# Kernel tuning notes

Measured on AMD Instinct MI355X. Metric: run time of the kernel, lower is better.

The kernel has to match this reference:

```python
import jax, jax.numpy as jnp
import numpy as np

N_PTS0 = 32   # sample points per line
N_PTS1 = 8    # after maxpool1d (kernel/stride = 4)
DIM_LOI = 128
DIM_FC = 1024
TOPK = 300
HW = 128
NLINES = 20000
NLAB = 3


def setup_inputs() -> dict:
    key = jax.random.key(0)
    ks = jax.random.split(key, 10)
    jloc = jax.random.uniform(ks[0], (1, HW, HW), dtype=jnp.float32)
    joff = jax.random.uniform(ks[1], (2, HW, HW), dtype=jnp.float32)
    loi_features = jax.random.normal(ks[2], (DIM_LOI, HW, HW), dtype=jnp.float32)
    edge_idx = jax.random.randint(ks[3], (NLINES, 2), 0, TOPK, dtype=jnp.int32)
    W1 = jax.random.normal(ks[4], (DIM_LOI * N_PTS1, DIM_FC), dtype=jnp.float32) * 0.02
    b1 = jnp.zeros((DIM_FC,), jnp.float32)
    W2 = jax.random.normal(ks[5], (DIM_FC, DIM_FC), dtype=jnp.float32) * 0.02
    b2 = jnp.zeros((DIM_FC,), jnp.float32)
    W3 = jax.random.normal(ks[6], (DIM_FC, NLAB), dtype=jnp.float32) * 0.02
    b3 = jnp.zeros((NLAB,), jnp.float32)
    return {"jloc": jloc, "joff": joff, "loi_features": loi_features,
            "edge_idx": edge_idx, "W1": W1, "b1": b1, "W2": W2, "b2": b2,
            "W3": W3, "b3": b3}


def reference(jloc, joff, loi_features, edge_idx, W1, b1, W2, b2, W3, b3):
    C, h, w = loi_features.shape
    # --- NMS: 3x3 max_pool2d, keep only local maxima ---
    ap = jax.lax.reduce_window(jloc, -jnp.inf, jax.lax.max,
                               (1, 3, 3), (1, 1, 1), 'SAME')
    jloc_nms = jloc * (jloc == ap).astype(jloc.dtype)
    # --- top-k junction decoding (joff_pred = sigmoid(joff) - 0.5) ---
    joff_pred = jax.nn.sigmoid(joff) - 0.5
    scores, idx = jax.lax.top_k(jloc_nms.reshape(-1), TOPK)
    joff_flat = joff_pred.reshape(2, -1)
    y = (idx // w).astype(jnp.float32) + joff_flat[1][idx] + 0.5
    x = (idx % w).astype(jnp.float32) + joff_flat[0][idx] + 0.5
    juncs = jnp.stack((x, y), axis=1)                       # [K, 2]
    # --- lines from junction pairs (lines_adjusted) ---
    lines = jnp.concatenate((juncs[edge_idx[:, 0]], juncs[edge_idx[:, 1]]), axis=1)  # [N, 4]
    # --- LOI pooling: bilinear sampling along each line ---
    tspan = jnp.linspace(0.0, 1.0, N_PTS0)                  # [P]
    U, V = lines[:, :2], lines[:, 2:]
    pts = U[:, :, None] * tspan + V[:, :, None] * (1.0 - tspan) - 0.5  # [N, 2, P]
    pts = pts.transpose(0, 2, 1).reshape(-1, 2)             # [N*P, 2]
    px, py = pts[:, 0], pts[:, 1]
    px0 = jnp.clip(jnp.floor(px), 0, w - 1)
    py0 = jnp.clip(jnp.floor(py), 0, h - 1)
    px1 = jnp.clip(px0 + 1, 0, w - 1)
    py1 = jnp.clip(py0 + 1, 0, h - 1)
    px0l, py0l = px0.astype(jnp.int32), py0.astype(jnp.int32)
    px1l, py1l = px1.astype(jnp.int32), py1.astype(jnp.int32)
    xp = (loi_features[:, py0l, px0l] * (py1 - py) * (px1 - px)
          + loi_features[:, py1l, px0l] * (py - py0) * (px1 - px)
          + loi_features[:, py0l, px1l] * (py1 - py) * (px - px0)
          + loi_features[:, py1l, px1l] * (py - py0) * (px - px0))  # [C, N*P]
    xp = xp.reshape(C, -1, N_PTS0).transpose(1, 0, 2)        # [N, C, P]
    k = N_PTS0 // N_PTS1
    xp = xp.reshape(xp.shape[0], C, N_PTS1, k).max(axis=-1)  # maxpool1d
    feats = xp.reshape(xp.shape[0], C * N_PTS1)              # [N, C*n_pts1]
    # --- fc2 MLP head ---
    h1 = jax.nn.relu(feats @ W1 + b1)
    h2 = jax.nn.relu(h1 @ W2 + b2)
    line_logits = h2 @ W3 + b3
    return line_logits
```

## Files before the change

kernel.cpp:

```cpp
#include <hip/hip_runtime.h>
#include <cmath>


typedef _Float16 f16;
typedef _Float16 f16x2 __attribute__((ext_vector_type(2)));
typedef _Float16 f16x8 __attribute__((ext_vector_type(8)));
typedef float f32x4 __attribute__((ext_vector_type(4)));

#define HWD 128
#define NPIX 16384
#define TOPK_N 300
#define NLINES 20000
#define MPAD 20096
#define KDIM 1024
#define NDIM 1024
#define MAXCAND 4096

#define G2L(gp, lp) __builtin_amdgcn_global_load_lds( \
    (const __attribute__((address_space(1))) void*)(gp), \
    (__attribute__((address_space(3))) void*)(lp), 16, 0, 0)

__global__ __launch_bounds__(256) void preproc_kernel(
    const float* __restrict__ loi, f16* __restrict__ loiT,
    const float* __restrict__ W1, f16* __restrict__ W1T,
    const float* __restrict__ W2, f16* __restrict__ W2T,
    const float* __restrict__ jloc, unsigned long long* __restrict__ cand,
    int* __restrict__ count, float* __restrict__ out, int out_n)
{
    const int bid = blockIdx.x;
    const int tid = threadIdx.x;
    if (bid < 128) {
        __shared__ f16 t[128 * 130];
        const int y = bid;
        #pragma unroll 4
        for (int it = 0; it < 64; ++it) {
            int idx = it * 256 + tid;
            int c = idx >> 7, x = idx & 127;
            t[x * 130 + c] = (f16)loi[c * NPIX + y * HWD + x];
        }
        __syncthreads();
        #pragma unroll
        for (int it = 0; it < 8; ++it) {
            int j = it * 256 + tid;
            int x = j >> 4, cc = (j & 15) * 8;
            f16x8 v;
            #pragma unroll
            for (int u = 0; u < 8; ++u) v[u] = t[x * 130 + cc + u];
            *(f16x8*)(loiT + (y * HWD + x) * HWD + cc) = v;
        }
    } else if (bid < 640) {
        const int b = bid - 128;
        const float* W = (b < 256) ? W1 : W2;
        f16* Wt = (b < 256) ? W1T : W2T;
        const int bb = b & 255;
        __shared__ f16 t[64 * 66];
        const int k0 = (bb >> 4) * 64;
        const int n0 = (bb & 15) * 64;
        #pragma unroll 4
        for (int it = 0; it < 16; ++it) {
            int i = it * 256 + tid;
            int r = i >> 6, c = i & 63;
            t[c * 66 + r] = (f16)W[(size_t)(k0 + r) * NDIM + n0 + c];
        }
        __syncthreads();
        #pragma unroll
        for (int it = 0; it < 2; ++it) {
            int j = it * 256 + tid;
            int nr = j >> 3, kc = (j & 7) * 8;
            f16x8 v;
            #pragma unroll
            for (int u = 0; u < 8; ++u) v[u] = t[nr * 66 + kc + u];
            const int kk = k0 + kc;
            *(f16x8*)(Wt + ((size_t)(kk >> 5) * NDIM + (n0 + nr)) * 32 + (kk & 31)) = v;
        }
    } else if (bid < 704) {
        const int p = (bid - 640) * 256 + tid;
        const int y = p >> 7, x = p & 127;
        const float c = jloc[p];
        float m = c;
        for (int dy = -1; dy <= 1; ++dy) {
            int yy = y + dy;
            if (yy < 0 || yy >= HWD) continue;
            for (int dx = -1; dx <= 1; ++dx) {
                int xx = x + dx;
                if (xx < 0 || xx >= HWD) continue;
                m = fmaxf(m, jloc[yy * HWD + xx]);
            }
        }
        if (c == m && c > 0.0f) {
            int pos = atomicAdd(count, 1);
            if (pos < MAXCAND) {
                unsigned int ub = __float_as_uint(c);
                cand[pos] = ((unsigned long long)ub << 32) |
                            (unsigned long long)(0xFFFFFFFFu - (unsigned int)p);
            }
        }
    } else {
        const int base = (bid - 704) * 1024 + tid * 4;
        #pragma unroll
        for (int u = 0; u < 4; ++u)
            if (base + u < out_n) out[base + u] = 0.f;
    }
}

__global__ __launch_bounds__(256) void rank_junc_kernel(
    const unsigned long long* __restrict__ cand, const int* __restrict__ count,
    const float* __restrict__ joff, float* __restrict__ juncs )
{
    __shared__ unsigned long long keys[MAXCAND];
    const int n = min(*count, MAXCAND);
    const int t = blockIdx.x * 256 + threadIdx.x;
    for (int i = threadIdx.x; i < n; i += 256)
        keys[i] = cand[i];
    __syncthreads();
    if (t >= n) return;
    const unsigned long long key = keys[t];
    int rank = 0;
    int j = 0;
    for (; j + 4 <= n; j += 4) {
        rank += (keys[j]     > key);
        rank += (keys[j + 1] > key);
        rank += (keys[j + 2] > key);
        rank += (keys[j + 3] > key);
    }
    for (; j < n; ++j) rank += (keys[j] > key);
    if (rank < TOPK_N) {
        unsigned int p = 0xFFFFFFFFu - (unsigned int)(key & 0xFFFFFFFFull);
        float sx = 1.0f / (1.0f + expf(-joff[p]));
        float sy = 1.0f / (1.0f + expf(-joff[NPIX + p]));
        juncs[2 * rank + 0] = (float)(p & 127) + sx;
        juncs[2 * rank + 1] = (float)(p >> 7) + sy;
    }
}

__global__ __launch_bounds__(256) void sample_kernel(
    const f16* __restrict__ loiT, const float* __restrict__ juncs,
    const int* __restrict__ edge_idx, f16* __restrict__ feats)
{
    const int wv = threadIdx.x >> 6;
    const int l = blockIdx.x * 4 + wv;
    const int lane = threadIdx.x & 63;

    __shared__ int   soff[4][32][4];
    __shared__ float swt[4][32][4];

    if (lane < 32) {
        const int e0 = edge_idx[2 * l], e1 = edge_idx[2 * l + 1];
        const float ux = juncs[2 * e0], uy = juncs[2 * e0 + 1];
        const float vx = juncs[2 * e1], vy = juncs[2 * e1 + 1];
        const int j = lane;
        const float t = (float)j * (1.0f / 31.0f);
        const float px = ux * t + vx * (1.0f - t) - 0.5f;
        const float py = uy * t + vy * (1.0f - t) - 0.5f;
        float fx0 = fminf(fmaxf(floorf(px), 0.0f), 127.0f);
        float fy0 = fminf(fmaxf(floorf(py), 0.0f), 127.0f);
        float fx1 = fminf(fx0 + 1.0f, 127.0f);
        float fy1 = fminf(fy0 + 1.0f, 127.0f);
        int ix0 = (int)fx0, iy0 = (int)fy0, ix1 = (int)fx1, iy1 = (int)fy1;
        soff[wv][j][0] = (iy0 * HWD + ix0) * HWD;
        soff[wv][j][1] = (iy1 * HWD + ix0) * HWD;
        soff[wv][j][2] = (iy0 * HWD + ix1) * HWD;
        soff[wv][j][3] = (iy1 * HWD + ix1) * HWD;
        swt[wv][j][0] = (fy1 - py) * (fx1 - px);
        swt[wv][j][1] = (py - fy0) * (fx1 - px);
        swt[wv][j][2] = (fy1 - py) * (px - fx0);
        swt[wv][j][3] = (py - fy0) * (px - fx0);
    }
    __syncthreads();

    const int c2 = lane * 2;
    f16x8 o0, o1;
    #pragma unroll
    for (int p = 0; p < 8; ++p) {
        float m0 = -INFINITY, m1 = -INFINITY;
        #pragma unroll
        for (int jj = 0; jj < 4; ++jj) {
            const int j = p * 4 + jj;
            const int b00 = soff[wv][j][0], b10 = soff[wv][j][1];
            const int b01 = soff[wv][j][2], b11 = soff[wv][j][3];
            const float w00 = swt[wv][j][0], w10 = swt[wv][j][1];
            const float w01 = swt[wv][j][2], w11 = swt[wv][j][3];
            f16x2 v00 = *(const f16x2*)(loiT + b00 + c2);
            f16x2 v10 = *(const f16x2*)(loiT + b10 + c2);
            f16x2 v01 = *(const f16x2*)(loiT + b01 + c2);
            f16x2 v11 = *(const f16x2*)(loiT + b11 + c2);
            float s0 = (float)v00.x * w00 + (float)v10.x * w10 +
                       (float)v01.x * w01 + (float)v11.x * w11;
            float s1 = (float)v00.y * w00 + (float)v10.y * w10 +
                       (float)v01.y * w01 + (float)v11.y * w11;
            m0 = fmaxf(m0, s0);
            m1 = fmaxf(m1, s1);
        }
        o0[p] = (f16)m0;
        o1[p] = (f16)m1;
    }
    f16* dst = feats + ((size_t)(lane >> 1) * MPAD + l) * 32 + (lane & 1) * 16;
    *(f16x8*)(dst) = o0;
    *(f16x8*)(dst + 8) = o1;
}

__global__ __launch_bounds__(256, 2) void gemm_bias_relu_kernel(
    const f16* __restrict__ A, const f16* __restrict__ Bt,
    const float* __restrict__ bias, f16* __restrict__ C,
    const float* __restrict__ W3, const float* __restrict__ b3,
    float* __restrict__ out, int K, int head)
{
    const int tid = threadIdx.x;
    const int wave = tid >> 6, lane = tid & 63;
    const int wm = wave >> 1, wn = wave & 1;
    const int m0 = blockIdx.y * 128;
    const int n0 = blockIdx.x * 256;

    __shared__ f16 sA0[128 * 32];
    __shared__ f16 sA1[128 * 32];
    __shared__ f16 sB0[256 * 32];
    __shared__ f16 sB1[256 * 32];

    f32x4 acc[4][8];
    #pragma unroll
    for (int mi = 0; mi < 4; ++mi)
        #pragma unroll
        for (int ni = 0; ni < 8; ++ni)
            acc[mi][ni] = (f32x4){0.f, 0.f, 0.f, 0.f};

    const size_t strideA = (size_t)MPAD * 32;
    const size_t strideB = (size_t)NDIM * 32;
    const f16* gA = A + (size_t)m0 * 32 + wave * 512 + lane * 8;
    const f16* gB = Bt + (size_t)n0 * 32 + wave * 512 + lane * 8;
    const int so = wave * 512;

    const int col16 = lane & 15;
    const int kq = (lane >> 4) * 8;

    const int NC = K >> 5;
    for (int c0 = 0; c0 < NC; c0 += 2) {
        const f16* a0 = gA + (size_t)c0 * strideA;
        const f16* a1 = a0 + strideA;
        const f16* b0 = gB + (size_t)c0 * strideB;
        const f16* b1 = b0 + strideB;
        __syncthreads();
        G2L(a0, sA0 + so);
        G2L(a0 + 2048, sA0 + so + 2048);
        G2L(a1, sA1 + so);
        G2L(a1 + 2048, sA1 + so + 2048);
        G2L(b0, sB0 + so);
        G2L(b0 + 2048, sB0 + so + 2048);
        G2L(b0 + 4096, sB0 + so + 4096);
        G2L(b0 + 6144, sB0 + so + 6144);
        G2L(b1, sB1 + so);
        G2L(b1 + 2048, sB1 + so + 2048);
        G2L(b1 + 4096, sB1 + so + 4096);
        G2L(b1 + 6144, sB1 + so + 6144);
        __builtin_amdgcn_s_waitcnt(0x0f70);
        __syncthreads();

        {
            f16x8 af[4], bf[8];
            #pragma unroll
            for (int i = 0; i < 4; ++i)
                af[i] = *(const f16x8*)(sA0 + (wm * 64 + i * 16 + col16) * 32 + kq);
            #pragma unroll
            for (int i = 0; i < 8; ++i)
                bf[i] = *(const f16x8*)(sB0 + (wn * 128 + i * 16 + col16) * 32 + kq);
            #pragma unroll
            for (int mi = 0; mi < 4; ++mi)
                #pragma unroll
                for (int ni = 0; ni < 8; ++ni)
                    acc[mi][ni] = __builtin_amdgcn_mfma_f32_16x16x32_f16(
                        af[mi], bf[ni], acc[mi][ni], 0, 0, 0);
        }
        {
            f16x8 af[4], bf[8];
            #pragma unroll
            for (int i = 0; i < 4; ++i)
                af[i] = *(const f16x8*)(sA1 + (wm * 64 + i * 16 + col16) * 32 + kq);
            #pragma unroll
            for (int i = 0; i < 8; ++i)
                bf[i] = *(const f16x8*)(sB1 + (wn * 128 + i * 16 + col16) * 32 + kq);
            #pragma unroll
            for (int mi = 0; mi < 4; ++mi)
                #pragma unroll
                for (int ni = 0; ni < 8; ++ni)
                    acc[mi][ni] = __builtin_amdgcn_mfma_f32_16x16x32_f16(
                        af[mi], bf[ni], acc[mi][ni], 0, 0, 0);
        }
    }

    const int quad = lane >> 4;
    if (!head) {
        #pragma unroll
        for (int ni = 0; ni < 8; ++ni) {
            const int n = n0 + wn * 128 + ni * 16 + col16;
            const float b = bias[n];
            const size_t cb = ((size_t)(n >> 5) * MPAD) * 32 + (n & 31);
            #pragma unroll
            for (int mi = 0; mi < 4; ++mi) {
                #pragma unroll
                for (int r = 0; r < 4; ++r) {
                    const int m = m0 + wm * 64 + mi * 16 + quad * 4 + r;
                    float v = fmaxf(acc[mi][ni][r] + b, 0.f);
                    C[cb + (size_t)m * 32] = (f16)v;
                }
            }
        }
    } else {
        float bb[8], w3c[8][3];
        #pragma unroll
        for (int ni = 0; ni < 8; ++ni) {
            const int n = n0 + wn * 128 + ni * 16 + col16;
            bb[ni] = bias[n];
            #pragma unroll
            for (int jj = 0; jj < 3; ++jj) w3c[ni][jj] = W3[n * 3 + jj];
        }
        const bool addb3 = (blockIdx.x == 0 && wn == 0);
        #pragma unroll
        for (int mi = 0; mi < 4; ++mi) {
            #pragma unroll
            for (int r = 0; r < 4; ++r) {
                float s0 = 0.f, s1 = 0.f, s2 = 0.f;
                #pragma unroll
                for (int ni = 0; ni < 8; ++ni) {
                    float v = fmaxf(acc[mi][ni][r] + bb[ni], 0.f);
                    s0 += v * w3c[ni][0];
                    s1 += v * w3c[ni][1];
                    s2 += v * w3c[ni][2];
                }
                #pragma unroll
                for (int mask = 1; mask <= 8; mask <<= 1) {
                    s0 += __shfl_xor(s0, mask);
                    s1 += __shfl_xor(s1, mask);
                    s2 += __shfl_xor(s2, mask);
                }
                if (col16 == 0) {
                    const int m = m0 + wm * 64 + mi * 16 + quad * 4 + r;
                    if (m < NLINES) {
                        atomicAdd(&out[m * 3 + 0], s0 + (addb3 ? b3[0] : 0.f));
                        atomicAdd(&out[m * 3 + 1], s1 + (addb3 ? b3[1] : 0.f));
                        atomicAdd(&out[m * 3 + 2], s2 + (addb3 ? b3[2] : 0.f));
                    }
                }
            }
        }
    }
}

extern "C" void kernel_launch(void* const* d_in, const int* in_sizes, int n_in,
                              void* d_out, int out_size, void* d_ws, size_t ws_size,
                              hipStream_t stream)
{
    const float* jloc = (const float*)d_in[0];
    const float* joff = (const float*)d_in[1];
    const float* loi  = (const float*)d_in[2];
    const int*   eidx = (const int*)d_in[3];
    const float* W1   = (const float*)d_in[4];
    const float* b1   = (const float*)d_in[5];
    const float* W2   = (const float*)d_in[6];
    const float* b2   = (const float*)d_in[7];
    const float* W3   = (const float*)d_in[8];
    const float* b3   = (const float*)d_in[9];
    float* out = (float*)d_out;

    char* ws = (char*)d_ws;
    f16*   loiT  = (f16*)(ws);
    f16*   W1T   = (f16*)(ws + ((size_t)4 << 20));
    f16*   W2T   = (f16*)(ws + ((size_t)6 << 20));
    float* juncs = (float*)(ws + ((size_t)8 << 20));
    int*   count = (int*)(ws + ((size_t)8 << 20) + 4096);
    unsigned long long* cand =
        (unsigned long long*)(ws + ((size_t)8 << 20) + 8192);
    f16*   feats = (f16*)(ws + ((size_t)9 << 20));
    f16*   h1    = (f16*)(ws + ((size_t)51 << 20));

    hipMemsetAsync(count, 0, sizeof(int), stream);
    preproc_kernel<<<dim3(764), dim3(256), 0, stream>>>(
        loi, loiT, W1, W1T, W2, W2T, jloc, cand, count, out, out_size);
    rank_junc_kernel<<<dim3(MAXCAND / 256), dim3(256), 0, stream>>>(
        cand, count, joff, juncs);
    sample_kernel<<<dim3(NLINES / 4), dim3(256), 0, stream>>>(loiT, juncs, eidx, feats);
    gemm_bias_relu_kernel<<<dim3(NDIM / 256, MPAD / 128), dim3(256), 0, stream>>>(
        feats, W1T, b1, h1, nullptr, nullptr, nullptr, KDIM, 0);
    gemm_bias_relu_kernel<<<dim3(NDIM / 256, MPAD / 128), dim3(256), 0, stream>>>(
        h1, W2T, b2, nullptr, W3, b3, out, KDIM, 1);
}
```

Before: 294.8 us.

## Triple-buffer GEMM LDS pipeline and XOR-swizzle operand layout to avoid bank conflicts

The GEMM main loop is replaced with a 3-stage ring buffer in dynamic LDS. Global-to-LDS loads for chunk c+2 are issued while chunk c is computed, with partial vmcnt waits and a single barrier per iteration, where before there was a full drain every two chunks. The layouts of feats, h1 and the transposed weights gain an XOR swizzle of 8-element octets keyed on row bits, so LDS fragment reads avoid bank conflicts. This raises LDS use to 72KB per block, which may reduce occupancy, and every producer and consumer layout must stay consistent.

```diff
diff --git a/kernel.cpp b/kernel.cpp
--- a/kernel.cpp
+++ b/kernel.cpp
@@ -15,6 +15,7 @@
 #define KDIM 1024
 #define NDIM 1024
 #define MAXCAND 4096
+
 
 #define G2L(gp, lp) __builtin_amdgcn_global_load_lds( \
     (const __attribute__((address_space(1))) void*)(gp), \
@@ -71,7 +72,9 @@
             #pragma unroll
             for (int u = 0; u < 8; ++u) v[u] = t[nr * 66 + kc + u];
             const int kk = k0 + kc;
-            *(f16x8*)(Wt + ((size_t)(kk >> 5) * NDIM + (n0 + nr)) * 32 + (kk & 31)) = v;
+            const int n = n0 + nr;
+            const int slot = ((kk >> 3) & 3) ^ ((n >> 1) & 3);
+            *(f16x8*)(Wt + ((size_t)(kk >> 5) * NDIM + n) * 32 + slot * 8) = v;
         }
     } else if (bid < 704) {
         const int p = (bid - 640) * 256 + tid;
@@ -194,9 +197,11 @@
         o0[p] = (f16)m0;
         o1[p] = (f16)m1;
     }
-    f16* dst = feats + ((size_t)(lane >> 1) * MPAD + l) * 32 + (lane & 1) * 16;
-    *(f16x8*)(dst) = o0;
-    *(f16x8*)(dst + 8) = o1;
+    const int rs = (l >> 1) & 3;
+    const int oct0 = (lane & 1) * 2;
+    f16* base = feats + ((size_t)(lane >> 1) * MPAD + l) * 32;
+    *(f16x8*)(base + ((oct0 ^ rs) * 8)) = o0;
+    *(f16x8*)(base + (((oct0 + 1) ^ rs) * 8)) = o1;
 }
 
 __global__ __launch_bounds__(256, 2) void gemm_bias_relu_kernel(
@@ -205,16 +210,16 @@
     const float* __restrict__ W3, const float* __restrict__ b3,
     float* __restrict__ out, int K, int head)
 {
+    extern __shared__ f16 lds[];
     const int tid = threadIdx.x;
     const int wave = tid >> 6, lane = tid & 63;
     const int wm = wave >> 1, wn = wave & 1;
     const int m0 = blockIdx.y * 128;
     const int n0 = blockIdx.x * 256;
 
-    __shared__ f16 sA0[128 * 32];
-    __shared__ f16 sA1[128 * 32];
-    __shared__ f16 sB0[256 * 32];
-    __shared__ f16 sB1[256 * 32];
+    const int col16 = lane & 15;
+    const int quad = lane >> 4;
+    const int swz = (quad ^ ((col16 >> 1) & 3)) * 8;
 
     f32x4 acc[4][8];
     #pragma unroll
@@ -226,80 +231,70 @@
     const size_t strideA = (size_t)MPAD * 32;
     const size_t strideB = (size_t)NDIM * 32;
     const f16* gA = A + (size_t)m0 * 32 + wave * 512 + lane * 8;
-    const f16* gB = Bt + (size_t)n0 * 32 + wave * 512 + lane * 8;
-    const int so = wave * 512;
-
-    const int col16 = lane & 15;
-    const int kq = (lane >> 4) * 8;
+    const f16* gB = Bt + (size_t)n0 * 32 + wave * 2048 + lane * 8;
+    const int sAo = wave * 512;
+    const int sBo = wave * 2048;
+
+#define STAGE(CN) do { \
+        f16* lb_ = lds + ((CN) % 3) * 12288; \
+        const f16* ga_ = gA + (size_t)(CN) * strideA; \
+        G2L(ga_,        lb_ + sAo); \
+        G2L(ga_ + 2048, lb_ + sAo + 2048); \
+        const f16* gb_ = gB + (size_t)(CN) * strideB; \
+        G2L(gb_,        lb_ + 4096 + sBo); \
+        G2L(gb_ + 512,  lb_ + 4096 + sBo + 512); \
+        G2L(gb_ + 1024, lb_ + 4096 + sBo + 1024); \
+        G2L(gb_ + 1536, lb_ + 4096 + sBo + 1536); \
+    } while (0)
+
+    STAGE(0);
+    asm volatile("" ::: "memory");
+    STAGE(1);
+    asm volatile("" ::: "memory");
 
     const int NC = K >> 5;
-    for (int c0 = 0; c0 < NC; c0 += 2) {
-        const f16* a0 = gA + (size_t)c0 * strideA;
-        const f16* a1 = a0 + strideA;
-        const f16* b0 = gB + (size_t)c0 * strideB;
-        const f16* b1 = b0 + strideB;
-        __syncthreads();
-        G2L(a0, sA0 + so);
-        G2L(a0 + 2048, sA0 + so + 2048);
-        G2L(a1, sA1 + so);
-        G2L(a1 + 2048, sA1 + so + 2048);
-        G2L(b0, sB0 + so);
-        G2L(b0 + 2048, sB0 + so + 2048);
-        G2L(b0 + 4096, sB0 + so + 4096);
-        G2L(b0 + 6144, sB0 + so + 6144);
-        G2L(b1, sB1 + so);
-        G2L(b1 + 2048, sB1 + so + 2048);
-        G2L(b1 + 4096, sB1 + so + 4096);
-        G2L(b1 + 6144, sB1 + so + 6144);
-        __builtin_amdgcn_s_waitcnt(0x0f70);
-        __syncthreads();
-
-        {
-            f16x8 af[4], bf[8];
-            #pragma unroll
-            for (int i = 0; i < 4; ++i)
-                af[i] = *(const f16x8*)(sA0 + (wm * 64 + i * 16 + col16) * 32 + kq);
-            #pragma unroll
-            for (int i = 0; i < 8; ++i)
-                bf[i] = *(const f16x8*)(sB0 + (wn * 128 + i * 16 + col16) * 32 + kq);
-            #pragma unroll
-            for (int mi = 0; mi < 4; ++mi)
-                #pragma unroll
-                for (int ni = 0; ni < 8; ++ni)
-                    acc[mi][ni] = __builtin_amdgcn_mfma_f32_16x16x32_f16(
-                        af[mi], bf[ni], acc[mi][ni], 0, 0, 0);
-        }
-        {
-            f16x8 af[4], bf[8];
-            #pragma unroll
-            for (int i = 0; i < 4; ++i)
-                af[i] = *(const f16x8*)(sA1 + (wm * 64 + i * 16 + col16) * 32 + kq);
-            #pragma unroll
-            for (int i = 0; i < 8; ++i)
-                bf[i] = *(const f16x8*)(sB1 + (wn * 128 + i * 16 + col16) * 32 + kq);
-            #pragma unroll
-            for (int mi = 0; mi < 4; ++mi)
-                #pragma unroll
-                for (int ni = 0; ni < 8; ++ni)
-                    acc[mi][ni] = __builtin_amdgcn_mfma_f32_16x16x32_f16(
-                        af[mi], bf[ni], acc[mi][ni], 0, 0, 0);
-        }
-    }
-
-    const int quad = lane >> 4;
+    for (int c = 0; c < NC; ++c) {
+        if (c + 1 < NC)
+            asm volatile("s_waitcnt vmcnt(6)" ::: "memory");
+        else
+            asm volatile("s_waitcnt vmcnt(0)" ::: "memory");
+        __builtin_amdgcn_s_barrier();
+        if (c + 2 < NC) STAGE(c + 2);
+        asm volatile("" ::: "memory");
+
+        const f16* buf = lds + (c % 3) * 12288;
+        const f16* pA = buf + (wm * 64 + col16) * 32 + swz;
+        const f16* pB = buf + 4096 + (wn * 128 + col16) * 32 + swz;
+        f16x8 af[4], bf[8];
+        #pragma unroll
+        for (int i = 0; i < 4; ++i)
+            af[i] = *(const f16x8*)(pA + i * 512);
+        #pragma unroll
+        for (int i = 0; i < 8; ++i)
+            bf[i] = *(const f16x8*)(pB + i * 512);
+        #pragma unroll
+        for (int mi = 0; mi < 4; ++mi)
+            #pragma unroll
+            for (int ni = 0; ni < 8; ++ni)
+                acc[mi][ni] = __builtin_amdgcn_mfma_f32_16x16x32_f16(
+                    af[mi], bf[ni], acc[mi][ni], 0, 0, 0);
+    }
+#undef STAGE
+
     if (!head) {
         #pragma unroll
         for (int ni = 0; ni < 8; ++ni) {
             const int n = n0 + wn * 128 + ni * 16 + col16;
             const float b = bias[n];
-            const size_t cb = ((size_t)(n >> 5) * MPAD) * 32 + (n & 31);
+            const size_t rb = (size_t)(n >> 5) * MPAD;
+            const int noct = (n >> 3) & 3, ne = n & 7;
             #pragma unroll
             for (int mi = 0; mi < 4; ++mi) {
                 #pragma unroll
                 for (int r = 0; r < 4; ++r) {
                     const int m = m0 + wm * 64 + mi * 16 + quad * 4 + r;
                     float v = fmaxf(acc[mi][ni][r] + b, 0.f);
-                    C[cb + (size_t)m * 32] = (f16)v;
+                    C[(rb + m) * 32 + ((noct ^ ((m >> 1) & 3)) * 8) + ne] = (f16)v;
                 }
             }
         }
@@ -371,14 +366,22 @@
     f16*   feats = (f16*)(ws + ((size_t)9 << 20));
     f16*   h1    = (f16*)(ws + ((size_t)51 << 20));
 
+    static int attr_done = 0;
+    if (!attr_done) {
+        (void)hipFuncSetAttribute(
+            reinterpret_cast<const void*>(&gemm_bias_relu_kernel),
+            hipFuncAttributeMaxDynamicSharedMemorySize, 73728);
+        attr_done = 1;
+    }
+
     hipMemsetAsync(count, 0, sizeof(int), stream);
     preproc_kernel<<<dim3(764), dim3(256), 0, stream>>>(
         loi, loiT, W1, W1T, W2, W2T, jloc, cand, count, out, out_size);
     rank_junc_kernel<<<dim3(MAXCAND / 256), dim3(256), 0, stream>>>(
         cand, count, joff, juncs);
     sample_kernel<<<dim3(NLINES / 4), dim3(256), 0, stream>>>(loiT, juncs, eidx, feats);
-    gemm_bias_relu_kernel<<<dim3(NDIM / 256, MPAD / 128), dim3(256), 0, stream>>>(
+    gemm_bias_relu_kernel<<<dim3(NDIM / 256, MPAD / 128), dim3(256), 73728, stream>>>(
         feats, W1T, b1, h1, nullptr, nullptr, nullptr, KDIM, 0);
-    gemm_bias_relu_kernel<<<dim3(NDIM / 256, MPAD / 128), dim3(256), 0, stream>>>(
+    gemm_bias_relu_kernel<<<dim3(NDIM / 256, MPAD / 128), dim3(256), 73728, stream>>>(
         h1, W2T, b2, nullptr, W3, b3, out, KDIM, 1);
 }
```

Result: no change. 292.4 us (-0.8%).
